# Kernel optimization log

Hardware: AMD Instinct MI355X
Metric: run time of the kernel (lower is better)

The kernel has to match this reference:

```python
import jax, jax.numpy as jnp
import numpy as np

N, E, D, H = 100000, 800000, 128, 4
DK = D // H
SCALE = 1.0 / np.sqrt(D)  # keep logits tame with random weights
EPS = 1e-5


def _layernorm(x, g, b):
    mu = jnp.mean(x, axis=-1, keepdims=True)
    var = jnp.mean(jnp.square(x - mu), axis=-1, keepdims=True)
    return (x - mu) * jax.lax.rsqrt(var + EPS) * g + b


def setup_inputs() -> dict:
    key = jax.random.key(0)
    ks = jax.random.split(key, 14)
    inp = {
        'h': jax.random.normal(ks[0], (N, D), jnp.float32),
        'e_ij': jax.random.normal(ks[1], (E, D), jnp.float32),
        'W1': jax.random.normal(ks[2], (D, D), jnp.float32) * SCALE,
        'W2': jax.random.normal(ks[3], (D, D), jnp.float32) * SCALE,
        'W3': jax.random.normal(ks[4], (D, D), jnp.float32) * SCALE,
        'W4': jax.random.normal(ks[5], (D, D), jnp.float32) * SCALE,
        'W5': jax.random.normal(ks[6], (D, D), jnp.float32) * SCALE,
        'W6': jax.random.normal(ks[7], (D, D), jnp.float32) * SCALE,
        'ln_gamma': jnp.ones((D,), jnp.float32),
        'ln_beta': jnp.zeros((D,), jnp.float32),
        'mlp_w1': jax.random.normal(ks[8], (D, 2 * D), jnp.float32) * SCALE,
        'mlp_w2': jax.random.normal(ks[9], (2 * D, D), jnp.float32) * (1.0 / np.sqrt(2 * D)),
        'src': jax.random.randint(ks[10], (E,), 0, N, jnp.int32),
        'dst': jax.random.randint(ks[11], (E,), 0, N, jnp.int32),
    }
    return inp


def reference(h, e_ij, W1, W2, W3, W4, W5, W6, ln_gamma, ln_beta, mlp_w1, mlp_w2, src, dst):
    u = (h @ W1).reshape(N, H, DK)      # src-side query
    v = (h @ W2).reshape(N, H, DK)      # dst-side
    x3 = (e_ij @ W3).reshape(E, H, DK)
    # m = v[dst] + x_ij ; attn = u[src] * m (elementwise per head/channel)
    m = v[dst] + x3                      # [E,H,DK]
    attn = (u[src] * m) / np.sqrt(DK)    # [E,H,DK]
    # edge_softmax: segment softmax over incoming edges of each dst node
    amax = jax.ops.segment_max(attn, dst, num_segments=N)   # [N,H,DK]
    ex = jnp.exp(attn - amax[dst])
    denom = jax.ops.segment_sum(ex, dst, num_segments=N)    # [N,H,DK]
    alpha = ex / denom[dst]
    k = (h @ W4).reshape(N, H, DK)
    x5 = (e_ij @ W5).reshape(E, H, DK)
    m2 = k[dst] + x5                     # [E,H,DK]
    agg = jax.ops.segment_sum(alpha * m2, dst, num_segments=N).reshape(N, D)
    h1 = h @ W6 + agg
    h1 = _layernorm(h1, ln_gamma, ln_beta)
    mlp_out = jax.nn.relu(h1 @ mlp_w1) @ mlp_w2
    h2 = _layernorm(h1 + mlp_out, ln_gamma, ln_beta)  # same LayerNorm params reused
    return h2
```

## Files before the change

kernel.cpp:

```cpp
#include <hip/hip_runtime.h>
#include <hip/hip_bf16.h>

#define N_NODES 100000
#define N_EDGES 800000

typedef __attribute__((ext_vector_type(8))) short short8v;
typedef __attribute__((ext_vector_type(4))) float f32x4;

__device__ __forceinline__ unsigned short f2bf(float f) {
    __hip_bfloat16 b = __float2bfloat16(f);
    return *(unsigned short*)&b;
}
__device__ __forceinline__ float bf2f(unsigned short u) {
    return __uint_as_float((unsigned)u << 16);
}
__device__ __forceinline__ unsigned pack2(float lo, float hi) {
    return (unsigned)f2bf(lo) | ((unsigned)f2bf(hi) << 16);
}

__global__ __launch_bounds__(256) void hist_dst(
    const int* __restrict__ dst, int* __restrict__ counts)
{
    int e = blockIdx.x * 256 + threadIdx.x;
    if (e < N_EDGES) atomicAdd(&counts[dst[e]], 1);
}

__global__ __launch_bounds__(256) void scan_p1(
    const int* __restrict__ in, int* __restrict__ partials, int n)
{
    __shared__ int ws[4];
    int t = threadIdx.x, lane = t & 63, wv = t >> 6;
    int base = blockIdx.x * 1024;
    int s = 0;
#pragma unroll
    for (int i = 0; i < 4; ++i) {
        int idx = base + i * 256 + t;
        s += (idx < n) ? in[idx] : 0;
    }
#pragma unroll
    for (int off = 1; off < 64; off <<= 1) s += __shfl_xor(s, off);
    if (lane == 0) ws[wv] = s;
    __syncthreads();
    if (t == 0) partials[blockIdx.x] = ws[0] + ws[1] + ws[2] + ws[3];
}

__global__ __launch_bounds__(64) void scan_p2(
    int* __restrict__ partials, int nb, int* __restrict__ total_out)
{
    int lane = threadIdx.x;
    int carry = 0;
    for (int base = 0; base < nb; base += 64) {
        int idx = base + lane;
        int v = (idx < nb) ? partials[idx] : 0;
        int s = v;
#pragma unroll
        for (int off = 1; off < 64; off <<= 1) {
            int w = __shfl_up(s, off);
            if (lane >= off) s += w;
        }
        if (idx < nb) partials[idx] = s - v + carry;
        carry += __shfl(s, 63);
    }
    if (lane == 0) *total_out = carry;
}

__global__ __launch_bounds__(256) void scan_p3(
    const int* __restrict__ in, int* __restrict__ out, int* __restrict__ cursor,
    const int* __restrict__ partials, int n)
{
    __shared__ int ws[4];
    __shared__ int wpre[4];
    __shared__ int s_tot;
    int t = threadIdx.x, lane = t & 63, wv = t >> 6;
    int base = blockIdx.x * 1024;
    int carry = partials[blockIdx.x];
    for (int sub = 0; sub < 4; ++sub) {
        int idx = base + sub * 256 + t;
        int v = (idx < n) ? in[idx] : 0;
        int s = v;
#pragma unroll
        for (int off = 1; off < 64; off <<= 1) {
            int w = __shfl_up(s, off);
            if (lane >= off) s += w;
        }
        if (lane == 63) ws[wv] = s;
        __syncthreads();
        if (t == 0) {
            int a = 0;
#pragma unroll
            for (int i = 0; i < 4; ++i) { wpre[i] = a; a += ws[i]; }
            s_tot = a;
        }
        __syncthreads();
        int excl = s - v + wpre[wv] + carry;
        if (idx < n) { out[idx] = excl; if (cursor) cursor[idx] = excl; }
        carry += s_tot;
        __syncthreads();
    }
}

__global__ __launch_bounds__(256) void scatter_edges(
    const int* __restrict__ dst, const int* __restrict__ src,
    int* __restrict__ cursor,
    int* __restrict__ edge_ord, int* __restrict__ src_ord,
    int* __restrict__ dst_ord)
{
    int e = blockIdx.x * 256 + threadIdx.x;
    if (e < N_EDGES) {
        int d = dst[e];
        int pos = atomicAdd(&cursor[d], 1);
        edge_ord[pos] = e;
        src_ord[pos] = src[e];
        dst_ord[pos] = d;
    }
}

__global__ __launch_bounds__(256) void calc_npieces(
    const int* __restrict__ offsets, int* __restrict__ npieces)
{
    int n = blockIdx.x * 256 + threadIdx.x;
    if (n < N_NODES) {
        int b = offsets[n], e = offsets[n + 1];
        npieces[n] = (e > b) ? (((e - 1) >> 6) - (b >> 6) + 1) : 0;
    }
}

__global__ __launch_bounds__(256) void prep_weights(
    const float* __restrict__ W1, const float* __restrict__ W2,
    const float* __restrict__ W3, const float* __restrict__ W4,
    const float* __restrict__ W5, const float* __restrict__ W6,
    const float* __restrict__ mw1, const float* __restrict__ mw2,
    unsigned short* __restrict__ w3t, unsigned short* __restrict__ w5t,
    unsigned short* __restrict__ wcatt,
    unsigned short* __restrict__ mw1t, unsigned short* __restrict__ mw2t)
{
    int bid = blockIdx.x;
    if (bid < 64) {
        int t = bid * 256 + threadIdx.x;
        int r = t >> 7, c = t & 127;
        w3t[c * 128 + r] = f2bf(W3[t]);
        w5t[c * 128 + r] = f2bf(W5[t]);
    } else if (bid < 320) {
        int t = (bid - 64) * 256 + threadIdx.x;
        int n = t >> 7, k = t & 127;
        const float* Wm = (n < 128) ? W1 : (n < 256) ? W2 : (n < 384) ? W4 : W6;
        wcatt[t] = f2bf(Wm[k * 128 + (n & 127)]);
    } else {
        int t = (bid - 320) * 256 + threadIdx.x;
        if (t < 32768) {
            int n = t >> 7, k = t & 127;
            mw1t[t] = f2bf(mw1[k * 256 + n]);
        } else {
            int s = t - 32768;
            int n = s >> 8, k = s & 255;
            mw2t[s] = f2bf(mw2[k * 128 + n]);
        }
    }
}

__global__ __launch_bounds__(256) void gemm_node(
    const float* __restrict__ A, const unsigned short* __restrict__ Bt,
    unsigned short* __restrict__ uvkb, float* __restrict__ hw6f)
{
    const int t = threadIdx.x;
    const int lane = t & 63, wv = t >> 6;
    const int l15 = lane & 15, kg = lane >> 4;
    const int m0 = blockIdx.x * 64;
    const int n0 = blockIdx.y * 128;
    const int M = N_NODES, K = 128;

    int arow = m0 + wv * 16 + l15;
    int arow_c = arow < M ? arow : M - 1;
    const float* ap = A + (size_t)arow_c * K + kg * 8;

    f32x4 acc[8];
#pragma unroll
    for (int nt = 0; nt < 8; ++nt) acc[nt] = (f32x4){0.f, 0.f, 0.f, 0.f};

    for (int ko = 0; ko < K; ko += 32) {
        float4 f0 = *(const float4*)(ap + ko);
        float4 f1 = *(const float4*)(ap + ko + 4);
        short8v af;
        af[0] = (short)f2bf(f0.x); af[1] = (short)f2bf(f0.y);
        af[2] = (short)f2bf(f0.z); af[3] = (short)f2bf(f0.w);
        af[4] = (short)f2bf(f1.x); af[5] = (short)f2bf(f1.y);
        af[6] = (short)f2bf(f1.z); af[7] = (short)f2bf(f1.w);
#pragma unroll
        for (int nt = 0; nt < 8; ++nt) {
            short8v bf = *(const short8v*)(Bt + (size_t)(n0 + nt * 16 + l15) * K + ko + kg * 8);
            acc[nt] = __builtin_amdgcn_mfma_f32_16x16x32_bf16(af, bf, acc[nt], 0, 0, 0);
        }
    }
#pragma unroll
    for (int nt = 0; nt < 8; ++nt) {
#pragma unroll
        for (int r = 0; r < 4; ++r) {
            int row = m0 + wv * 16 + kg * 4 + r;
            if (row < M) {
                int col = n0 + nt * 16 + l15;
                float vfl = acc[nt][r];
                if (n0 < 384) uvkb[(size_t)row * 384 + col] = f2bf(vfl);
                else          hw6f[(size_t)row * 128 + col - 384] = vfl;
            }
        }
    }
}

__global__ __launch_bounds__(256) void gemm_bf16(
    const unsigned short* __restrict__ A, const unsigned short* __restrict__ Bt,
    int M, int K, int Nc,
    const float* __restrict__ res, float* __restrict__ Cf,
    unsigned short* __restrict__ Cb, int do_relu)
{
    const int t = threadIdx.x;
    const int lane = t & 63, wv = t >> 6;
    const int l15 = lane & 15, kg = lane >> 4;
    const int m0 = blockIdx.x * 64;
    const int n0 = blockIdx.y * 128;

    int arow = m0 + wv * 16 + l15;
    int arow_c = arow < M ? arow : M - 1;
    const unsigned short* ap = A + (size_t)arow_c * K + kg * 8;

    f32x4 acc[8];
#pragma unroll
    for (int nt = 0; nt < 8; ++nt) acc[nt] = (f32x4){0.f, 0.f, 0.f, 0.f};

    for (int ko = 0; ko < K; ko += 32) {
        short8v af = *(const short8v*)(ap + ko);
#pragma unroll
        for (int nt = 0; nt < 8; ++nt) {
            short8v bf = *(const short8v*)(Bt + (size_t)(n0 + nt * 16 + l15) * K + ko + kg * 8);
            acc[nt] = __builtin_amdgcn_mfma_f32_16x16x32_bf16(af, bf, acc[nt], 0, 0, 0);
        }
    }
#pragma unroll
    for (int nt = 0; nt < 8; ++nt) {
#pragma unroll
        for (int r = 0; r < 4; ++r) {
            int row = m0 + wv * 16 + kg * 4 + r;
            if (row < M) {
                int col = n0 + nt * 16 + l15;
                float vfl = acc[nt][r];
                if (res) vfl += res[(size_t)row * Nc + col];
                if (do_relu) vfl = fmaxf(vfl, 0.f);
                if (Cf) Cf[(size_t)row * Nc + col] = vfl;
                else    Cb[(size_t)row * Nc + col] = f2bf(vfl);
            }
        }
    }
}

__global__ __launch_bounds__(256) void gemm_bf16_ln(
    const unsigned short* __restrict__ A, const unsigned short* __restrict__ Bt,
    int M, int K, const float* __restrict__ res,
    const float* __restrict__ gamma, const float* __restrict__ beta,
    float* __restrict__ out)
{
    const int t = threadIdx.x;
    const int lane = t & 63, wv = t >> 6;
    const int l15 = lane & 15, kg = lane >> 4;
    const int m0 = blockIdx.x * 64;

    int arow = m0 + wv * 16 + l15;
    int arow_c = arow < M ? arow : M - 1;
    const unsigned short* ap = A + (size_t)arow_c * K + kg * 8;

    f32x4 acc[8];
#pragma unroll
    for (int nt = 0; nt < 8; ++nt) acc[nt] = (f32x4){0.f, 0.f, 0.f, 0.f};

    for (int ko = 0; ko < K; ko += 32) {
        short8v af = *(const short8v*)(ap + ko);
#pragma unroll
        for (int nt = 0; nt < 8; ++nt) {
            short8v bf = *(const short8v*)(Bt + (size_t)(nt * 16 + l15) * K + ko + kg * 8);
            acc[nt] = __builtin_amdgcn_mfma_f32_16x16x32_bf16(af, bf, acc[nt], 0, 0, 0);
        }
    }

    float gv[8], bv[8];
#pragma unroll
    for (int nt = 0; nt < 8; ++nt) {
        gv[nt] = gamma[nt * 16 + l15];
        bv[nt] = beta[nt * 16 + l15];
    }

#pragma unroll
    for (int r = 0; r < 4; ++r) {
        int row = m0 + wv * 16 + kg * 4 + r;
        int rc = row < M ? row : M - 1;
        float x[8];
        float s = 0.f;
#pragma unroll
        for (int nt = 0; nt < 8; ++nt) {
            x[nt] = acc[nt][r] + res[(size_t)rc * 128 + nt * 16 + l15];
            s += x[nt];
        }
#pragma unroll
        for (int off = 1; off < 16; off <<= 1) s += __shfl_xor(s, off);
        float mu = s * (1.f / 128.f);
        float ss = 0.f;
#pragma unroll
        for (int nt = 0; nt < 8; ++nt) {
            float d = x[nt] - mu;
            ss += d * d;
        }
#pragma unroll
        for (int off = 1; off < 16; off <<= 1) ss += __shfl_xor(ss, off);
        float rsv = rsqrtf(ss * (1.f / 128.f) + 1e-5f);
        if (row < M) {
#pragma unroll
            for (int nt = 0; nt < 8; ++nt)
                out[(size_t)row * 128 + nt * 16 + l15] =
                    (x[nt] - mu) * rsv * gv[nt] + bv[nt];
        }
    }
}

__global__ __launch_bounds__(256) void edge_agg(
    const float* __restrict__ e_ij,
    const unsigned short* __restrict__ w3t, const unsigned short* __restrict__ w5t,
    const unsigned short* __restrict__ uvkb,
    const int* __restrict__ edge_ord, const int* __restrict__ src_ord,
    const int* __restrict__ dst_ord,
    const int* __restrict__ offsets, const int* __restrict__ ppos,
    float* __restrict__ dpart, float* __restrict__ apart)
{
    __shared__ unsigned short e_s[64 * 136];
    __shared__ unsigned short u_s[64 * 136];
    __shared__ int s_eid[64], s_src[64], s_dst[64];
    __shared__ int s_sb[64], s_se[64], s_pi[64];
    __shared__ int s_nseg;
    const int t  = threadIdx.x;
    const int e0 = blockIdx.x * 64;

    if (t < 64) {
        s_eid[t] = edge_ord[e0 + t];
        s_src[t] = src_ord[e0 + t];
        int d = dst_ord[e0 + t];
        s_dst[t] = d;
        int dprev = __shfl_up(d, 1);
        bool bnd = (t == 0) || (d != dprev);
        unsigned long long mask = __ballot(bnd);
        int sid = __popcll(mask & ((1ull << t) - 1ull));
        if (bnd) {
            s_sb[sid] = t;
            s_pi[sid] = ppos[d] + (int)blockIdx.x - (offsets[d] >> 6);
            if (t > 0) s_se[sid - 1] = t;
        }
        if (t == 63) {
            int ns = __popcll(mask);
            s_se[ns - 1] = 64;
            s_nseg = ns;
        }
    }
    __syncthreads();
#pragma unroll
    for (int i = 0; i < 4; ++i) {
        int flat = t + i * 256;
        int row = flat >> 4, c8 = (flat & 15) * 8;
        const float* p = &e_ij[(size_t)s_eid[row] * 128 + c8];
        float4 f0 = *(const float4*)p;
        float4 f1 = *(const float4*)(p + 4);
        short8v uv = *(const short8v*)(uvkb + (size_t)s_src[row] * 384 + c8);
        short8v pk;
        pk[0] = (short)f2bf(f0.x); pk[1] = (short)f2bf(f0.y);
        pk[2] = (short)f2bf(f0.z); pk[3] = (short)f2bf(f0.w);
        pk[4] = (short)f2bf(f1.x); pk[5] = (short)f2bf(f1.y);
        pk[6] = (short)f2bf(f1.z); pk[7] = (short)f2bf(f1.w);
        *(short8v*)(e_s + row * 136 + c8) = pk;
        *(short8v*)(u_s + row * 136 + c8) = uv;
    }
    __syncthreads();

    const int lane = t & 63, wv = t >> 6;
    const int l15 = lane & 15, kg = lane >> 4;
    const int cb = wv * 32 + 2 * l15;

    const float inv = 0.17677669529663687f;
    const int nseg = __builtin_amdgcn_readfirstlane(s_nseg);
    float ex0[4][4], ex1[4][4];

    {
        const unsigned short* b3p0 = w3t + (size_t)(cb + 0) * 128 + kg * 8;
        const unsigned short* b3p1 = w3t + (size_t)(cb + 1) * 128 + kg * 8;
        f32x4 a3[4][2];
#pragma unroll
        for (int m = 0; m < 4; ++m) {
            a3[m][0] = (f32x4){0.f, 0.f, 0.f, 0.f};
            a3[m][1] = (f32x4){0.f, 0.f, 0.f, 0.f};
        }
#pragma unroll
        for (int kidx = 0; kidx < 4; ++kidx) {
            const int ko = kidx * 32;
            short8v b30 = *(const short8v*)(b3p0 + ko);
            short8v b31 = *(const short8v*)(b3p1 + ko);
#pragma unroll
            for (int m = 0; m < 4; ++m) {
                short8v af = *(const short8v*)(e_s + (m * 16 + l15) * 136 + kg * 8 + ko);
                a3[m][0] = __builtin_amdgcn_mfma_f32_16x16x32_bf16(af, b30, a3[m][0], 0, 0, 0);
                a3[m][1] = __builtin_amdgcn_mfma_f32_16x16x32_bf16(af, b31, a3[m][1], 0, 0, 0);
            }
        }
#pragma unroll
        for (int m = 0; m < 4; ++m) {
#pragma unroll
            for (int r = 0; r < 4; ++r) {
                int le = m * 16 + kg * 4 + r;
                int d  = s_dst[le];
                unsigned upk = *(const unsigned*)(u_s + (size_t)le * 136 + cb);
                unsigned vpk = *(const unsigned*)&uvkb[(size_t)d * 384 + 128 + cb];
                float u0 = bf2f((unsigned short)(upk & 0xffffu));
                float u1 = bf2f((unsigned short)(upk >> 16));
                float v0 = bf2f((unsigned short)(vpk & 0xffffu));
                float v1 = bf2f((unsigned short)(vpk >> 16));
                float at0 = u0 * (v0 + a3[m][0][r]) * inv;
                float at1 = u1 * (v1 + a3[m][1][r]) * inv;
                ex0[m][r] = __expf(fminf(at0, 80.f));
                ex1[m][r] = __expf(fminf(at1, 80.f));
            }
        }
    }
    f32x4 a5[4][2];
    {
        const unsigned short* b5p0 = w5t + (size_t)(cb + 0) * 128 + kg * 8;
        const unsigned short* b5p1 = w5t + (size_t)(cb + 1) * 128 + kg * 8;
#pragma unroll
        for (int m = 0; m < 4; ++m) {
            a5[m][0] = (f32x4){0.f, 0.f, 0.f, 0.f};
            a5[m][1] = (f32x4){0.f, 0.f, 0.f, 0.f};
        }
#pragma unroll
        for (int kidx = 0; kidx < 4; ++kidx) {
            const int ko = kidx * 32;
            short8v b50 = *(const short8v*)(b5p0 + ko);
            short8v b51 = *(const short8v*)(b5p1 + ko);
#pragma unroll
            for (int m = 0; m < 4; ++m) {
                short8v af = *(const short8v*)(e_s + (m * 16 + l15) * 136 + kg * 8 + ko);
                a5[m][0] = __builtin_amdgcn_mfma_f32_16x16x32_bf16(af, b50, a5[m][0], 0, 0, 0);
                a5[m][1] = __builtin_amdgcn_mfma_f32_16x16x32_bf16(af, b51, a5[m][1], 0, 0, 0);
            }
        }
#pragma unroll
        for (int m = 0; m < 4; ++m) {
#pragma unroll
            for (int r = 0; r < 4; ++r) {
                a5[m][0][r] = ex0[m][r] * a5[m][0][r];
                a5[m][1][r] = ex1[m][r] * a5[m][1][r];
            }
        }
    }
    for (int sg = 0; sg < nseg; ++sg) {
        const int b  = __builtin_amdgcn_readfirstlane(s_sb[sg]);
        const int e2 = __builtin_amdgcn_readfirstlane(s_se[sg]);
        const int pi = __builtin_amdgcn_readfirstlane(s_pi[sg]);
        float d0 = 0.f, d1 = 0.f, g0 = 0.f, g1 = 0.f;
#pragma unroll
        for (int m = 0; m < 4; ++m) {
            if (b < m * 16 + 16 && e2 > m * 16) {
#pragma unroll
                for (int r = 0; r < 4; ++r) {
                    int slot = m * 16 + kg * 4 + r;
                    bool in = (slot >= b) && (slot < e2);
                    d0 += in ? ex0[m][r] : 0.f;
                    d1 += in ? ex1[m][r] : 0.f;
                    g0 += in ? a5[m][0][r] : 0.f;
                    g1 += in ? a5[m][1][r] : 0.f;
                }
            }
        }
        d0 += __shfl_xor(d0, 16); d0 += __shfl_xor(d0, 32);
        d1 += __shfl_xor(d1, 16); d1 += __shfl_xor(d1, 32);
        g0 += __shfl_xor(g0, 16); g0 += __shfl_xor(g0, 32);
        g1 += __shfl_xor(g1, 16); g1 += __shfl_xor(g1, 32);
        if (kg == 0) {
            *(float2*)&dpart[(size_t)pi * 128 + cb] = make_float2(d0, d1);
            *(float2*)&apart[(size_t)pi * 128 + cb] = make_float2(g0, g1);
        }
    }
}

__global__ __launch_bounds__(256) void node_finalize(
    const float* __restrict__ hw6f, const unsigned short* __restrict__ uvkb,
    const float* __restrict__ dpart, const float* __restrict__ apart,
    const int* __restrict__ ppos,
    const float* __restrict__ gamma, const float* __restrict__ beta,
    float* __restrict__ h1, unsigned short* __restrict__ h1b)
{
    int n = blockIdx.x * 4 + (threadIdx.x >> 6);
    int lane = threadIdx.x & 63;
    int p0 = ppos[n], p1 = ppos[n + 1];
    float de0 = 0.f, de1 = 0.f, g0 = 0.f, g1 = 0.f;
    for (int j = p0; j < p1; ++j) {
        float2 dv = *(const float2*)&dpart[(size_t)j * 128 + lane * 2];
        float2 av = *(const float2*)&apart[(size_t)j * 128 + lane * 2];
        de0 += dv.x; de1 += dv.y;
        g0  += av.x; g1  += av.y;
    }
    unsigned kpk = *(const unsigned*)&uvkb[(size_t)n * 384 + 256 + lane * 2];
    float k0 = bf2f((unsigned short)(kpk & 0xffffu));
    float k1 = bf2f((unsigned short)(kpk >> 16));
    float2 hw = *(const float2*)&hw6f[(size_t)n * 128 + lane * 2];
    float x0 = hw.x + (de0 > 0.f ? k0 + g0 / de0 : 0.f);
    float x1 = hw.y + (de1 > 0.f ? k1 + g1 / de1 : 0.f);
    float s = x0 + x1;
#pragma unroll
    for (int off = 1; off < 64; off <<= 1) s += __shfl_xor(s, off);
    float mu = s * (1.f / 128.f);
    float d0 = x0 - mu, d1 = x1 - mu;
    float ss = d0 * d0 + d1 * d1;
#pragma unroll
    for (int off = 1; off < 64; off <<= 1) ss += __shfl_xor(ss, off);
    float rs = rsqrtf(ss * (1.f / 128.f) + 1e-5f);
    float2 g = *(const float2*)&gamma[lane * 2];
    float2 b = *(const float2*)&beta[lane * 2];
    float o0 = d0 * rs * g.x + b.x;
    float o1 = d1 * rs * g.y + b.y;
    size_t base = (size_t)n * 128 + lane * 2;
    *(float2*)&h1[base] = make_float2(o0, o1);
    *(unsigned*)&h1b[base] = pack2(o0, o1);
}

extern "C" void kernel_launch(void* const* d_in, const int* in_sizes, int n_in,
                              void* d_out, int out_size, void* d_ws, size_t ws_size,
                              hipStream_t stream)
{
    const float* h    = (const float*)d_in[0];
    const float* e_ij = (const float*)d_in[1];
    const float* W1   = (const float*)d_in[2];
    const float* W2   = (const float*)d_in[3];
    const float* W3   = (const float*)d_in[4];
    const float* W4   = (const float*)d_in[5];
    const float* W5   = (const float*)d_in[6];
    const float* W6   = (const float*)d_in[7];
    const float* ln_g = (const float*)d_in[8];
    const float* ln_b = (const float*)d_in[9];
    const float* mw1  = (const float*)d_in[10];
    const float* mw2  = (const float*)d_in[11];
    const int*   src  = (const int*)d_in[12];
    const int*   dst  = (const int*)d_in[13];
    float* out = (float*)d_out;

    float* ws = (float*)d_ws;
    float* hw6f  = ws;
    float* h1    = ws + 12800000;
    float* dpart = ws + 25600000;
    float* apart = ws + 40100000;
    unsigned short* uvkb    = (unsigned short*)(ws + 54600000);
    unsigned short* h1b     = (unsigned short*)(ws + 73800000);
    unsigned short* hiddenb = (unsigned short*)(ws + 80200000);
    unsigned short* w3t   = (unsigned short*)(ws + 93000000);
    unsigned short* w5t   = w3t + 16384;
    unsigned short* wcatt = w5t + 16384;
    unsigned short* mw1t  = wcatt + 65536;
    unsigned short* mw2t  = mw1t + 32768;
    int* ibase    = (int*)(ws + 93100000);
    int* counts   = ibase;
    int* offsets  = ibase + 100000;
    int* cursor   = ibase + 200001;
    int* npieces  = ibase + 300001;
    int* ppos     = ibase + 400001;
    int* partials = ibase + 500102;
    int* edge_ord = ibase + 500230;
    int* src_ord  = edge_ord + N_EDGES;
    int* dst_ord  = src_ord + N_EDGES;

    dim3 blk(256);
    hipMemsetAsync(counts, 0, N_NODES * sizeof(int), stream);

    hist_dst<<<N_EDGES / 256, blk, 0, stream>>>(dst, counts);
    scan_p1<<<98, blk, 0, stream>>>(counts, partials, N_NODES);
    scan_p2<<<1, 64, 0, stream>>>(partials, 98, offsets + N_NODES);
    scan_p3<<<98, blk, 0, stream>>>(counts, offsets, cursor, partials, N_NODES);
    scatter_edges<<<N_EDGES / 256, blk, 0, stream>>>(dst, src, cursor,
                                                     edge_ord, src_ord, dst_ord);
    calc_npieces<<<391, blk, 0, stream>>>(offsets, npieces);
    scan_p1<<<98, blk, 0, stream>>>(npieces, partials, N_NODES);
    scan_p2<<<1, 64, 0, stream>>>(partials, 98, ppos + N_NODES);
    scan_p3<<<98, blk, 0, stream>>>(npieces, ppos, (int*)nullptr, partials, N_NODES);

    prep_weights<<<576, blk, 0, stream>>>(W1, W2, W3, W4, W5, W6, mw1, mw2,
                                          w3t, w5t, wcatt, mw1t, mw2t);

    gemm_node<<<dim3(1563, 4), blk, 0, stream>>>(h, wcatt, uvkb, hw6f);

    edge_agg<<<N_EDGES / 64, blk, 0, stream>>>(e_ij, w3t, w5t, uvkb,
                                               edge_ord, src_ord, dst_ord,
                                               offsets, ppos, dpart, apart);

    node_finalize<<<N_NODES / 4, blk, 0, stream>>>(hw6f, uvkb, dpart, apart, ppos,
                                                   ln_g, ln_b, h1, h1b);

    gemm_bf16<<<dim3(1563, 2), blk, 0, stream>>>(h1b, mw1t, N_NODES, 128, 256,
                                                 nullptr, nullptr, hiddenb, 1);
    gemm_bf16_ln<<<1563, blk, 0, stream>>>(hiddenb, mw2t, N_NODES, 256,
                                           h1, ln_g, ln_b, out);
}
```

Measured before the change: 708.4 us.

## Make edge_agg persistent with double-buffered e_ij prefetch across edge tiles

Changes edge_agg from one block per 64-edge tile to 2500 persistent blocks that each loop over 5 tiles. The next tile's e_ij rows are prefetched into registers during the W3 MFMA and written to a second LDS buffer, and edge metadata is staged two tiles ahead in a triple buffer. The u_s staging is dropped, so u values are gathered directly from global memory per element, and launch bounds now request 4 blocks per CU. The goal is to hide gather latency behind compute. The cost is more register pressure from the prefetch registers and uncoalesced u loads.

```diff
diff --git a/kernel.cpp b/kernel.cpp
--- a/kernel.cpp
+++ b/kernel.cpp
@@ -3,6 +3,8 @@
 
 #define N_NODES 100000
 #define N_EDGES 800000
+#define EDGE_GRID 2500
+#define EDGE_SLOTS 5
 
 typedef __attribute__((ext_vector_type(8))) short short8v;
 typedef __attribute__((ext_vector_type(4))) float f32x4;
@@ -318,7 +320,7 @@
     }
 }
 
-__global__ __launch_bounds__(256) void edge_agg(
+__global__ __launch_bounds__(256, 4) void edge_agg(
     const float* __restrict__ e_ij,
     const unsigned short* __restrict__ w3t, const unsigned short* __restrict__ w5t,
     const unsigned short* __restrict__ uvkb,
@@ -327,158 +329,223 @@
     const int* __restrict__ offsets, const int* __restrict__ ppos,
     float* __restrict__ dpart, float* __restrict__ apart)
 {
-    __shared__ unsigned short e_s[64 * 136];
-    __shared__ unsigned short u_s[64 * 136];
-    __shared__ int s_eid[64], s_src[64], s_dst[64];
-    __shared__ int s_sb[64], s_se[64], s_pi[64];
-    __shared__ int s_nseg;
+    __shared__ unsigned short e_s[2][64 * 136];
+    __shared__ int s_eid[3][64], s_src[3][64], s_dst[3][64];
+    __shared__ int s_sb[3][64], s_se[3][64], s_pi[3][64];
+    __shared__ int s_nseg[3];
+
     const int t  = threadIdx.x;
-    const int e0 = blockIdx.x * 64;
+    const int lane = t & 63, wv = t >> 6;
+    const int l15 = lane & 15, kg = lane >> 4;
+    const int cb = wv * 32 + 2 * l15;
+    const float inv = 0.17677669529663687f;
+    const int b0 = blockIdx.x;
 
     if (t < 64) {
-        s_eid[t] = edge_ord[e0 + t];
-        s_src[t] = src_ord[e0 + t];
-        int d = dst_ord[e0 + t];
-        s_dst[t] = d;
-        int dprev = __shfl_up(d, 1);
-        bool bnd = (t == 0) || (d != dprev);
-        unsigned long long mask = __ballot(bnd);
-        int sid = __popcll(mask & ((1ull << t) - 1ull));
-        if (bnd) {
-            s_sb[sid] = t;
-            s_pi[sid] = ppos[d] + (int)blockIdx.x - (offsets[d] >> 6);
-            if (t > 0) s_se[sid - 1] = t;
-        }
-        if (t == 63) {
-            int ns = __popcll(mask);
-            s_se[ns - 1] = 64;
-            s_nseg = ns;
+        for (int j = 0; j < 2; ++j) {
+            int slot = b0 + j * EDGE_GRID;
+            int e0 = slot * 64;
+            int eid = edge_ord[e0 + t];
+            int sv  = src_ord[e0 + t];
+            int d   = dst_ord[e0 + t];
+            s_eid[j][t] = eid; s_src[j][t] = sv; s_dst[j][t] = d;
+            int dprev = __shfl_up(d, 1);
+            bool bnd = (t == 0) || (d != dprev);
+            unsigned long long mask = __ballot(bnd);
+            int sid = __popcll(mask & ((1ull << t) - 1ull));
+            if (bnd) {
+                s_sb[j][sid] = t;
+                s_pi[j][sid] = ppos[d] + slot - (offsets[d] >> 6);
+                if (t > 0) s_se[j][sid - 1] = t;
+            }
+            if (t == 63) {
+                int ns = __popcll(mask);
+                s_se[j][ns - 1] = 64;
+                s_nseg[j] = ns;
+            }
         }
     }
     __syncthreads();
+
 #pragma unroll
     for (int i = 0; i < 4; ++i) {
         int flat = t + i * 256;
         int row = flat >> 4, c8 = (flat & 15) * 8;
-        const float* p = &e_ij[(size_t)s_eid[row] * 128 + c8];
+        const float* p = &e_ij[(size_t)s_eid[0][row] * 128 + c8];
         float4 f0 = *(const float4*)p;
         float4 f1 = *(const float4*)(p + 4);
-        short8v uv = *(const short8v*)(uvkb + (size_t)s_src[row] * 384 + c8);
         short8v pk;
         pk[0] = (short)f2bf(f0.x); pk[1] = (short)f2bf(f0.y);
         pk[2] = (short)f2bf(f0.z); pk[3] = (short)f2bf(f0.w);
         pk[4] = (short)f2bf(f1.x); pk[5] = (short)f2bf(f1.y);
         pk[6] = (short)f2bf(f1.z); pk[7] = (short)f2bf(f1.w);
-        *(short8v*)(e_s + row * 136 + c8) = pk;
-        *(short8v*)(u_s + row * 136 + c8) = uv;
+        *(short8v*)(&e_s[0][row * 136 + c8]) = pk;
     }
     __syncthreads();
 
-    const int lane = t & 63, wv = t >> 6;
-    const int l15 = lane & 15, kg = lane >> 4;
-    const int cb = wv * 32 + 2 * l15;
-
-    const float inv = 0.17677669529663687f;
-    const int nseg = __builtin_amdgcn_readfirstlane(s_nseg);
-    float ex0[4][4], ex1[4][4];
-
-    {
-        const unsigned short* b3p0 = w3t + (size_t)(cb + 0) * 128 + kg * 8;
-        const unsigned short* b3p1 = w3t + (size_t)(cb + 1) * 128 + kg * 8;
-        f32x4 a3[4][2];
-#pragma unroll
-        for (int m = 0; m < 4; ++m) {
-            a3[m][0] = (f32x4){0.f, 0.f, 0.f, 0.f};
-            a3[m][1] = (f32x4){0.f, 0.f, 0.f, 0.f};
-        }
-#pragma unroll
-        for (int kidx = 0; kidx < 4; ++kidx) {
-            const int ko = kidx * 32;
-            short8v b30 = *(const short8v*)(b3p0 + ko);
-            short8v b31 = *(const short8v*)(b3p1 + ko);
+    for (int it = 0; it < EDGE_SLOTS; ++it) {
+        const int cur = it & 1;
+        const int mi  = it % 3;
+        const int mi1 = (it + 1) % 3;
+        const int mi2 = (it + 2) % 3;
+
+        float4 pre[8];
+        if (it < EDGE_SLOTS - 1) {
+#pragma unroll
+            for (int i = 0; i < 4; ++i) {
+                int flat = t + i * 256;
+                int row = flat >> 4, c8 = (flat & 15) * 8;
+                const float* p = &e_ij[(size_t)s_eid[mi1][row] * 128 + c8];
+                pre[2 * i]     = *(const float4*)p;
+                pre[2 * i + 1] = *(const float4*)(p + 4);
+            }
+        }
+        int m_eid = 0, m_src = 0, m_dst = 0;
+        if (t < 64 && it < EDGE_SLOTS - 2) {
+            int e0 = (b0 + (it + 2) * EDGE_GRID) * 64;
+            m_eid = edge_ord[e0 + t];
+            m_src = src_ord[e0 + t];
+            m_dst = dst_ord[e0 + t];
+        }
+
+        const int nseg = __builtin_amdgcn_readfirstlane(s_nseg[mi]);
+        float ex0[4][4], ex1[4][4];
+
+        {
+            const unsigned short* b3p0 = w3t + (size_t)(cb + 0) * 128 + kg * 8;
+            const unsigned short* b3p1 = w3t + (size_t)(cb + 1) * 128 + kg * 8;
+            f32x4 a3[4][2];
 #pragma unroll
             for (int m = 0; m < 4; ++m) {
-                short8v af = *(const short8v*)(e_s + (m * 16 + l15) * 136 + kg * 8 + ko);
-                a3[m][0] = __builtin_amdgcn_mfma_f32_16x16x32_bf16(af, b30, a3[m][0], 0, 0, 0);
-                a3[m][1] = __builtin_amdgcn_mfma_f32_16x16x32_bf16(af, b31, a3[m][1], 0, 0, 0);
-            }
-        }
-#pragma unroll
-        for (int m = 0; m < 4; ++m) {
-#pragma unroll
-            for (int r = 0; r < 4; ++r) {
-                int le = m * 16 + kg * 4 + r;
-                int d  = s_dst[le];
-                unsigned upk = *(const unsigned*)(u_s + (size_t)le * 136 + cb);
-                unsigned vpk = *(const unsigned*)&uvkb[(size_t)d * 384 + 128 + cb];
-                float u0 = bf2f((unsigned short)(upk & 0xffffu));
-                float u1 = bf2f((unsigned short)(upk >> 16));
-                float v0 = bf2f((unsigned short)(vpk & 0xffffu));
-                float v1 = bf2f((unsigned short)(vpk >> 16));
-                float at0 = u0 * (v0 + a3[m][0][r]) * inv;
-                float at1 = u1 * (v1 + a3[m][1][r]) * inv;
-                ex0[m][r] = __expf(fminf(at0, 80.f));
-                ex1[m][r] = __expf(fminf(at1, 80.f));
-            }
-        }
-    }
-    f32x4 a5[4][2];
-    {
-        const unsigned short* b5p0 = w5t + (size_t)(cb + 0) * 128 + kg * 8;
-        const unsigned short* b5p1 = w5t + (size_t)(cb + 1) * 128 + kg * 8;
-#pragma unroll
-        for (int m = 0; m < 4; ++m) {
-            a5[m][0] = (f32x4){0.f, 0.f, 0.f, 0.f};
-            a5[m][1] = (f32x4){0.f, 0.f, 0.f, 0.f};
-        }
-#pragma unroll
-        for (int kidx = 0; kidx < 4; ++kidx) {
-            const int ko = kidx * 32;
-            short8v b50 = *(const short8v*)(b5p0 + ko);
-            short8v b51 = *(const short8v*)(b5p1 + ko);
+                a3[m][0] = (f32x4){0.f, 0.f, 0.f, 0.f};
+                a3[m][1] = (f32x4){0.f, 0.f, 0.f, 0.f};
+            }
+#pragma unroll
+            for (int kidx = 0; kidx < 4; ++kidx) {
+                const int ko = kidx * 32;
+                short8v b30 = *(const short8v*)(b3p0 + ko);
+                short8v b31 = *(const short8v*)(b3p1 + ko);
+#pragma unroll
+                for (int m = 0; m < 4; ++m) {
+                    short8v af = *(const short8v*)(&e_s[cur][(m * 16 + l15) * 136 + kg * 8 + ko]);
+                    a3[m][0] = __builtin_amdgcn_mfma_f32_16x16x32_bf16(af, b30, a3[m][0], 0, 0, 0);
+                    a3[m][1] = __builtin_amdgcn_mfma_f32_16x16x32_bf16(af, b31, a3[m][1], 0, 0, 0);
+                }
+            }
 #pragma unroll
             for (int m = 0; m < 4; ++m) {
-                short8v af = *(const short8v*)(e_s + (m * 16 + l15) * 136 + kg * 8 + ko);
-                a5[m][0] = __builtin_amdgcn_mfma_f32_16x16x32_bf16(af, b50, a5[m][0], 0, 0, 0);
-                a5[m][1] = __builtin_amdgcn_mfma_f32_16x16x32_bf16(af, b51, a5[m][1], 0, 0, 0);
-            }
-        }
-#pragma unroll
-        for (int m = 0; m < 4; ++m) {
-#pragma unroll
-            for (int r = 0; r < 4; ++r) {
-                a5[m][0][r] = ex0[m][r] * a5[m][0][r];
-                a5[m][1][r] = ex1[m][r] * a5[m][1][r];
-            }
-        }
-    }
-    for (int sg = 0; sg < nseg; ++sg) {
-        const int b  = __builtin_amdgcn_readfirstlane(s_sb[sg]);
-        const int e2 = __builtin_amdgcn_readfirstlane(s_se[sg]);
-        const int pi = __builtin_amdgcn_readfirstlane(s_pi[sg]);
-        float d0 = 0.f, d1 = 0.f, g0 = 0.f, g1 = 0.f;
-#pragma unroll
-        for (int m = 0; m < 4; ++m) {
-            if (b < m * 16 + 16 && e2 > m * 16) {
 #pragma unroll
                 for (int r = 0; r < 4; ++r) {
-                    int slot = m * 16 + kg * 4 + r;
-                    bool in = (slot >= b) && (slot < e2);
-                    d0 += in ? ex0[m][r] : 0.f;
-                    d1 += in ? ex1[m][r] : 0.f;
-                    g0 += in ? a5[m][0][r] : 0.f;
-                    g1 += in ? a5[m][1][r] : 0.f;
+                    int le = m * 16 + kg * 4 + r;
+                    int d  = s_dst[mi][le];
+                    int sv = s_src[mi][le];
+                    unsigned upk = *(const unsigned*)&uvkb[(size_t)sv * 384 + cb];
+                    unsigned vpk = *(const unsigned*)&uvkb[(size_t)d * 384 + 128 + cb];
+                    float u0 = bf2f((unsigned short)(upk & 0xffffu));
+                    float u1 = bf2f((unsigned short)(upk >> 16));
+                    float v0 = bf2f((unsigned short)(vpk & 0xffffu));
+                    float v1 = bf2f((unsigned short)(vpk >> 16));
+                    float at0 = u0 * (v0 + a3[m][0][r]) * inv;
+                    float at1 = u1 * (v1 + a3[m][1][r]) * inv;
+                    ex0[m][r] = __expf(fminf(at0, 80.f));
+                    ex1[m][r] = __expf(fminf(at1, 80.f));
                 }
             }
         }
-        d0 += __shfl_xor(d0, 16); d0 += __shfl_xor(d0, 32);
-        d1 += __shfl_xor(d1, 16); d1 += __shfl_xor(d1, 32);
-        g0 += __shfl_xor(g0, 16); g0 += __shfl_xor(g0, 32);
-        g1 += __shfl_xor(g1, 16); g1 += __shfl_xor(g1, 32);
-        if (kg == 0) {
-            *(float2*)&dpart[(size_t)pi * 128 + cb] = make_float2(d0, d1);
-            *(float2*)&apart[(size_t)pi * 128 + cb] = make_float2(g0, g1);
-        }
+
+        if (it < EDGE_SLOTS - 1) {
+#pragma unroll
+            for (int i = 0; i < 4; ++i) {
+                int flat = t + i * 256;
+                int row = flat >> 4, c8 = (flat & 15) * 8;
+                short8v pk;
+                pk[0] = (short)f2bf(pre[2 * i].x);     pk[1] = (short)f2bf(pre[2 * i].y);
+                pk[2] = (short)f2bf(pre[2 * i].z);     pk[3] = (short)f2bf(pre[2 * i].w);
+                pk[4] = (short)f2bf(pre[2 * i + 1].x); pk[5] = (short)f2bf(pre[2 * i + 1].y);
+                pk[6] = (short)f2bf(pre[2 * i + 1].z); pk[7] = (short)f2bf(pre[2 * i + 1].w);
+                *(short8v*)(&e_s[cur ^ 1][row * 136 + c8]) = pk;
+            }
+        }
+
+        f32x4 a5[4][2];
+        {
+            const unsigned short* b5p0 = w5t + (size_t)(cb + 0) * 128 + kg * 8;
+            const unsigned short* b5p1 = w5t + (size_t)(cb + 1) * 128 + kg * 8;
+#pragma unroll
+            for (int m = 0; m < 4; ++m) {
+                a5[m][0] = (f32x4){0.f, 0.f, 0.f, 0.f};
+                a5[m][1] = (f32x4){0.f, 0.f, 0.f, 0.f};
+            }
+#pragma unroll
+            for (int kidx = 0; kidx < 4; ++kidx) {
+                const int ko = kidx * 32;
+                short8v b50 = *(const short8v*)(b5p0 + ko);
+                short8v b51 = *(const short8v*)(b5p1 + ko);
+#pragma unroll
+                for (int m = 0; m < 4; ++m) {
+                    short8v af = *(const short8v*)(&e_s[cur][(m * 16 + l15) * 136 + kg * 8 + ko]);
+                    a5[m][0] = __builtin_amdgcn_mfma_f32_16x16x32_bf16(af, b50, a5[m][0], 0, 0, 0);
+                    a5[m][1] = __builtin_amdgcn_mfma_f32_16x16x32_bf16(af, b51, a5[m][1], 0, 0, 0);
+                }
+            }
+#pragma unroll
+            for (int m = 0; m < 4; ++m) {
+#pragma unroll
+                for (int r = 0; r < 4; ++r) {
+                    a5[m][0][r] = ex0[m][r] * a5[m][0][r];
+                    a5[m][1][r] = ex1[m][r] * a5[m][1][r];
+                }
+            }
+        }
+
+        for (int sg = 0; sg < nseg; ++sg) {
+            const int b  = __builtin_amdgcn_readfirstlane(s_sb[mi][sg]);
+            const int e2 = __builtin_amdgcn_readfirstlane(s_se[mi][sg]);
+            const int pi = __builtin_amdgcn_readfirstlane(s_pi[mi][sg]);
+            float d0 = 0.f, d1 = 0.f, g0 = 0.f, g1 = 0.f;
+#pragma unroll
+            for (int m = 0; m < 4; ++m) {
+                if (b < m * 16 + 16 && e2 > m * 16) {
+#pragma unroll
+                    for (int r = 0; r < 4; ++r) {
+                        int slot = m * 16 + kg * 4 + r;
+                        bool in = (slot >= b) && (slot < e2);
+                        d0 += in ? ex0[m][r] : 0.f;
+                        d1 += in ? ex1[m][r] : 0.f;
+                        g0 += in ? a5[m][0][r] : 0.f;
+                        g1 += in ? a5[m][1][r] : 0.f;
+                    }
+                }
+            }
+            d0 += __shfl_xor(d0, 16); d0 += __shfl_xor(d0, 32);
+            d1 += __shfl_xor(d1, 16); d1 += __shfl_xor(d1, 32);
+            g0 += __shfl_xor(g0, 16); g0 += __shfl_xor(g0, 32);
+            g1 += __shfl_xor(g1, 16); g1 += __shfl_xor(g1, 32);
+            if (kg == 0) {
+                *(float2*)&dpart[(size_t)pi * 128 + cb] = make_float2(d0, d1);
+                *(float2*)&apart[(size_t)pi * 128 + cb] = make_float2(g0, g1);
+            }
+        }
+
+        if (t < 64 && it < EDGE_SLOTS - 2) {
+            int slot2 = b0 + (it + 2) * EDGE_GRID;
+            s_eid[mi2][t] = m_eid; s_src[mi2][t] = m_src; s_dst[mi2][t] = m_dst;
+            int dprev = __shfl_up(m_dst, 1);
+            bool bnd = (t == 0) || (m_dst != dprev);
+            unsigned long long mask = __ballot(bnd);
+            int sid = __popcll(mask & ((1ull << t) - 1ull));
+            if (bnd) {
+                s_sb[mi2][sid] = t;
+                s_pi[mi2][sid] = ppos[m_dst] + slot2 - (offsets[m_dst] >> 6);
+                if (t > 0) s_se[mi2][sid - 1] = t;
+            }
+            if (t == 63) {
+                int ns = __popcll(mask);
+                s_se[mi2][ns - 1] = 64;
+                s_nseg[mi2] = ns;
+            }
+        }
+        __syncthreads();
     }
 }
 
@@ -586,9 +653,9 @@
 
     gemm_node<<<dim3(1563, 4), blk, 0, stream>>>(h, wcatt, uvkb, hw6f);
 
-    edge_agg<<<N_EDGES / 64, blk, 0, stream>>>(e_ij, w3t, w5t, uvkb,
-                                               edge_ord, src_ord, dst_ord,
-                                               offsets, ppos, dpart, apart);
+    edge_agg<<<EDGE_GRID, blk, 0, stream>>>(e_ij, w3t, w5t, uvkb,
+                                            edge_ord, src_ord, dst_ord,
+                                            offsets, ppos, dpart, apart);
 
     node_finalize<<<N_NODES / 4, blk, 0, stream>>>(hw6f, uvkb, dpart, apart, ppos,
                                                    ln_g, ln_b, h1, h1b);
```

New measurement: 1.122 ms. 58.4% more time.

## Load edge features directly into MFMA fragments and fuse W3/W5 GEMM loops

Applied to the files above, without the earlier changes.

Removes the shared-memory staging of the gathered e_ij rows and u[src] rows, along with one block barrier. Each wave now loads its A fragments straight from global memory, converts them to bf16 in registers, and feeds them to a single fused loop that does both the W3 and W5 MFMAs. The u values are gathered from global memory per output element instead of from LDS. This cuts LDS footprint and barrier cost, but each of the four waves now re-reads the same e_ij rows from global/L2, so e_ij load traffic rises about fourfold, and register pressure goes up.

```diff
diff --git a/kernel.cpp b/kernel.cpp
--- a/kernel.cpp
+++ b/kernel.cpp
@@ -327,8 +327,6 @@
     const int* __restrict__ offsets, const int* __restrict__ ppos,
     float* __restrict__ dpart, float* __restrict__ apart)
 {
-    __shared__ unsigned short e_s[64 * 136];
-    __shared__ unsigned short u_s[64 * 136];
     __shared__ int s_eid[64], s_src[64], s_dst[64];
     __shared__ int s_sb[64], s_se[64], s_pi[64];
     __shared__ int s_nseg;
@@ -356,23 +354,6 @@
         }
     }
     __syncthreads();
-#pragma unroll
-    for (int i = 0; i < 4; ++i) {
-        int flat = t + i * 256;
-        int row = flat >> 4, c8 = (flat & 15) * 8;
-        const float* p = &e_ij[(size_t)s_eid[row] * 128 + c8];
-        float4 f0 = *(const float4*)p;
-        float4 f1 = *(const float4*)(p + 4);
-        short8v uv = *(const short8v*)(uvkb + (size_t)s_src[row] * 384 + c8);
-        short8v pk;
-        pk[0] = (short)f2bf(f0.x); pk[1] = (short)f2bf(f0.y);
-        pk[2] = (short)f2bf(f0.z); pk[3] = (short)f2bf(f0.w);
-        pk[4] = (short)f2bf(f1.x); pk[5] = (short)f2bf(f1.y);
-        pk[6] = (short)f2bf(f1.z); pk[7] = (short)f2bf(f1.w);
-        *(short8v*)(e_s + row * 136 + c8) = pk;
-        *(short8v*)(u_s + row * 136 + c8) = uv;
-    }
-    __syncthreads();
 
     const int lane = t & 63, wv = t >> 6;
     const int l15 = lane & 15, kg = lane >> 4;
@@ -380,78 +361,73 @@
 
     const float inv = 0.17677669529663687f;
     const int nseg = __builtin_amdgcn_readfirstlane(s_nseg);
-    float ex0[4][4], ex1[4][4];
-
+
+    int eid[4];
+#pragma unroll
+    for (int m = 0; m < 4; ++m) eid[m] = s_eid[m * 16 + l15];
+
+    f32x4 a3[4][2], a5[4][2];
+#pragma unroll
+    for (int m = 0; m < 4; ++m) {
+        a3[m][0] = (f32x4){0.f, 0.f, 0.f, 0.f};
+        a3[m][1] = (f32x4){0.f, 0.f, 0.f, 0.f};
+        a5[m][0] = (f32x4){0.f, 0.f, 0.f, 0.f};
+        a5[m][1] = (f32x4){0.f, 0.f, 0.f, 0.f};
+    }
     {
         const unsigned short* b3p0 = w3t + (size_t)(cb + 0) * 128 + kg * 8;
         const unsigned short* b3p1 = w3t + (size_t)(cb + 1) * 128 + kg * 8;
-        f32x4 a3[4][2];
-#pragma unroll
-        for (int m = 0; m < 4; ++m) {
-            a3[m][0] = (f32x4){0.f, 0.f, 0.f, 0.f};
-            a3[m][1] = (f32x4){0.f, 0.f, 0.f, 0.f};
-        }
+        const unsigned short* b5p0 = w5t + (size_t)(cb + 0) * 128 + kg * 8;
+        const unsigned short* b5p1 = w5t + (size_t)(cb + 1) * 128 + kg * 8;
 #pragma unroll
         for (int kidx = 0; kidx < 4; ++kidx) {
             const int ko = kidx * 32;
             short8v b30 = *(const short8v*)(b3p0 + ko);
             short8v b31 = *(const short8v*)(b3p1 + ko);
+            short8v b50 = *(const short8v*)(b5p0 + ko);
+            short8v b51 = *(const short8v*)(b5p1 + ko);
 #pragma unroll
             for (int m = 0; m < 4; ++m) {
-                short8v af = *(const short8v*)(e_s + (m * 16 + l15) * 136 + kg * 8 + ko);
+                const float* p = e_ij + (size_t)eid[m] * 128 + ko + kg * 8;
+                float4 f0 = *(const float4*)p;
+                float4 f1 = *(const float4*)(p + 4);
+                short8v af;
+                af[0] = (short)f2bf(f0.x); af[1] = (short)f2bf(f0.y);
+                af[2] = (short)f2bf(f0.z); af[3] = (short)f2bf(f0.w);
+                af[4] = (short)f2bf(f1.x); af[5] = (short)f2bf(f1.y);
+                af[6] = (short)f2bf(f1.z); af[7] = (short)f2bf(f1.w);
                 a3[m][0] = __builtin_amdgcn_mfma_f32_16x16x32_bf16(af, b30, a3[m][0], 0, 0, 0);
                 a3[m][1] = __builtin_amdgcn_mfma_f32_16x16x32_bf16(af, b31, a3[m][1], 0, 0, 0);
-            }
-        }
-#pragma unroll
-        for (int m = 0; m < 4; ++m) {
-#pragma unroll
-            for (int r = 0; r < 4; ++r) {
-                int le = m * 16 + kg * 4 + r;
-                int d  = s_dst[le];
-                unsigned upk = *(const unsigned*)(u_s + (size_t)le * 136 + cb);
-                unsigned vpk = *(const unsigned*)&uvkb[(size_t)d * 384 + 128 + cb];
-                float u0 = bf2f((unsigned short)(upk & 0xffffu));
-                float u1 = bf2f((unsigned short)(upk >> 16));
-                float v0 = bf2f((unsigned short)(vpk & 0xffffu));
-                float v1 = bf2f((unsigned short)(vpk >> 16));
-                float at0 = u0 * (v0 + a3[m][0][r]) * inv;
-                float at1 = u1 * (v1 + a3[m][1][r]) * inv;
-                ex0[m][r] = __expf(fminf(at0, 80.f));
-                ex1[m][r] = __expf(fminf(at1, 80.f));
-            }
-        }
-    }
-    f32x4 a5[4][2];
-    {
-        const unsigned short* b5p0 = w5t + (size_t)(cb + 0) * 128 + kg * 8;
-        const unsigned short* b5p1 = w5t + (size_t)(cb + 1) * 128 + kg * 8;
-#pragma unroll
-        for (int m = 0; m < 4; ++m) {
-            a5[m][0] = (f32x4){0.f, 0.f, 0.f, 0.f};
-            a5[m][1] = (f32x4){0.f, 0.f, 0.f, 0.f};
-        }
-#pragma unroll
-        for (int kidx = 0; kidx < 4; ++kidx) {
-            const int ko = kidx * 32;
-            short8v b50 = *(const short8v*)(b5p0 + ko);
-            short8v b51 = *(const short8v*)(b5p1 + ko);
-#pragma unroll
-            for (int m = 0; m < 4; ++m) {
-                short8v af = *(const short8v*)(e_s + (m * 16 + l15) * 136 + kg * 8 + ko);
                 a5[m][0] = __builtin_amdgcn_mfma_f32_16x16x32_bf16(af, b50, a5[m][0], 0, 0, 0);
                 a5[m][1] = __builtin_amdgcn_mfma_f32_16x16x32_bf16(af, b51, a5[m][1], 0, 0, 0);
             }
         }
-#pragma unroll
-        for (int m = 0; m < 4; ++m) {
-#pragma unroll
-            for (int r = 0; r < 4; ++r) {
-                a5[m][0][r] = ex0[m][r] * a5[m][0][r];
-                a5[m][1][r] = ex1[m][r] * a5[m][1][r];
-            }
-        }
-    }
+    }
+
+#pragma unroll
+    for (int m = 0; m < 4; ++m) {
+#pragma unroll
+        for (int r = 0; r < 4; ++r) {
+            int le = m * 16 + kg * 4 + r;
+            int d  = s_dst[le];
+            int sv = s_src[le];
+            unsigned upk = *(const unsigned*)&uvkb[(size_t)sv * 384 + cb];
+            unsigned vpk = *(const unsigned*)&uvkb[(size_t)d * 384 + 128 + cb];
+            float u0 = bf2f((unsigned short)(upk & 0xffffu));
+            float u1 = bf2f((unsigned short)(upk >> 16));
+            float v0 = bf2f((unsigned short)(vpk & 0xffffu));
+            float v1 = bf2f((unsigned short)(vpk >> 16));
+            float at0 = u0 * (v0 + a3[m][0][r]) * inv;
+            float at1 = u1 * (v1 + a3[m][1][r]) * inv;
+            float ex0 = __expf(fminf(at0, 80.f));
+            float ex1 = __expf(fminf(at1, 80.f));
+            a3[m][0][r] = ex0;
+            a3[m][1][r] = ex1;
+            a5[m][0][r] = ex0 * a5[m][0][r];
+            a5[m][1][r] = ex1 * a5[m][1][r];
+        }
+    }
+
     for (int sg = 0; sg < nseg; ++sg) {
         const int b  = __builtin_amdgcn_readfirstlane(s_sb[sg]);
         const int e2 = __builtin_amdgcn_readfirstlane(s_se[sg]);
@@ -464,8 +440,8 @@
                 for (int r = 0; r < 4; ++r) {
                     int slot = m * 16 + kg * 4 + r;
                     bool in = (slot >= b) && (slot < e2);
-                    d0 += in ? ex0[m][r] : 0.f;
-                    d1 += in ? ex1[m][r] : 0.f;
+                    d0 += in ? a3[m][0][r] : 0.f;
+                    d1 += in ? a3[m][1][r] : 0.f;
                     g0 += in ? a5[m][0][r] : 0.f;
                     g1 += in ? a5[m][1][r] : 0.f;
                 }
```

New measurement: 921.3 us. +30.0%, slower.
